# Performance work log

Measured on AMD Instinct MI355X. Metric: run time of the kernel, lower is better.

## Reference

```python
import jax, jax.numpy as jnp
import numpy as np
from jax import lax

# Fixed image shape (H, W) for all images, standard detection resize
H_IMG, W_IMG = 800.0, 1333.0
SCORE_THRESH = 0.05
NMS_THRESH = 0.5
DET_PER_IMG = 100
K_PRE = 2048  # NMS candidate budget per image (after score threshold)
BBOX_XFORM_CLIP = float(np.log(1000.0 / 16.0))
WX, WY, WW, WH = 10.0, 10.0, 5.0, 5.0  # bbox_reg_weights


def setup_inputs() -> dict:
    B, P, C = 8, 2000, 81
    key = jax.random.key(0)
    k1, k2, k3, k4 = jax.random.split(key, 4)
    class_logits = 2.0 * jax.random.normal(k1, (B * P, C), jnp.float32)
    box_regression = 0.5 * jax.random.normal(k2, (B * P, C * 4), jnp.float32)
    # valid proposal boxes inside the image: (x1,y1) + (w,h)
    xy = jax.random.uniform(k3, (B, P, 2), jnp.float32) * jnp.array([W_IMG - 128.0, H_IMG - 128.0], jnp.float32)
    wh = 1.0 + 127.0 * jax.random.uniform(k4, (B, P, 2), jnp.float32)
    proposals = jnp.concatenate([xy, xy + wh], axis=-1)
    return {"class_logits": class_logits, "box_regression": box_regression, "proposals": proposals}


def _decode(rel, boxes):
    # BoxCoder.decode: rel [N, C, 4], boxes [N, 4] -> [N, C, 4]
    w = boxes[:, 2] - boxes[:, 0]
    h = boxes[:, 3] - boxes[:, 1]
    cx = boxes[:, 0] + 0.5 * w
    cy = boxes[:, 1] + 0.5 * h
    dx = rel[..., 0] / WX
    dy = rel[..., 1] / WY
    dw = jnp.minimum(rel[..., 2] / WW, BBOX_XFORM_CLIP)
    dh = jnp.minimum(rel[..., 3] / WH, BBOX_XFORM_CLIP)
    pcx = dx * w[:, None] + cx[:, None]
    pcy = dy * h[:, None] + cy[:, None]
    pw = jnp.exp(dw) * w[:, None]
    ph = jnp.exp(dh) * h[:, None]
    return jnp.stack([pcx - 0.5 * pw, pcy - 0.5 * ph, pcx + 0.5 * pw, pcy + 0.5 * ph], axis=-1)


def _pairwise_iou(b):
    # b: [K, 4] -> [K, K]
    area = jnp.maximum(b[:, 2] - b[:, 0], 0.0) * jnp.maximum(b[:, 3] - b[:, 1], 0.0)
    lt = jnp.maximum(b[:, None, :2], b[None, :, :2])
    rb = jnp.minimum(b[:, None, 2:], b[None, :, 2:])
    wh = jnp.maximum(rb - lt, 0.0)
    inter = wh[..., 0] * wh[..., 1]
    union = area[:, None] + area[None, :] - inter
    return inter / jnp.maximum(union, 1e-9)


def _greedy_nms(boxes, valid):
    # boxes: [K, 4] sorted by score desc; valid: [K] bool. Exact greedy NMS.
    K = boxes.shape[0]
    iou = _pairwise_iou(boxes)
    idx = jnp.arange(K)

    def body(i, keep):
        sup = keep[i] & (iou[i] > NMS_THRESH) & (idx > i)
        return keep & ~sup

    return lax.fori_loop(0, K, body, valid)


def reference(class_logits, box_regression, proposals):
    B, P, _ = proposals.shape
    C = class_logits.shape[-1]
    # decode all class-specific boxes, softmax scores
    rel = box_regression.reshape(-1, C, 4)
    pred = _decode(rel, proposals.reshape(-1, 4)).reshape(B, P, C, 4)
    scores = jax.nn.softmax(class_logits, axis=-1).reshape(B, P, C)
    # drop background class 0
    M = P * (C - 1)
    boxes = pred[:, :, 1:, :].reshape(B, M, 4)
    scores = scores[:, :, 1:].reshape(B, M)
    labels = jnp.broadcast_to(jnp.arange(1, C)[None, None, :], (B, P, C - 1)).reshape(B, M)
    # clip to image
    x1 = jnp.clip(boxes[..., 0], 0.0, W_IMG)
    y1 = jnp.clip(boxes[..., 1], 0.0, H_IMG)
    x2 = jnp.clip(boxes[..., 2], 0.0, W_IMG)
    y2 = jnp.clip(boxes[..., 3], 0.0, H_IMG)
    boxes = jnp.stack([x1, y1, x2, y2], axis=-1)
    # score threshold + remove_small_boxes(min_size=0.01), as a validity mask
    valid = (scores > SCORE_THRESH) & ((x2 - x1) >= 0.01) & ((y2 - y1) >= 0.01)
    masked = jnp.where(valid, scores, -1.0)
    # top-K candidates per image (sorted desc -> NMS visiting order)
    top_s, top_i = lax.top_k(masked, K_PRE)
    top_b = jnp.take_along_axis(boxes, top_i[..., None], axis=1)
    top_l = jnp.take_along_axis(labels, top_i, axis=1)
    top_v = top_s > 0.0
    # batched_nms: per-class coordinate offsets so classes never overlap
    off = top_l.astype(jnp.float32) * (jnp.maximum(W_IMG, H_IMG) + 1.0)
    keep = jax.vmap(_greedy_nms)(top_b + off[..., None], top_v)
    final = jnp.where(keep, top_s, -1.0)
    det_s, det_i = lax.top_k(final, DET_PER_IMG)
    det_b = jnp.take_along_axis(top_b, det_i[..., None], axis=1)
    det_l = jnp.take_along_axis(top_l, det_i, axis=1)
    det_valid = det_s > 0.0  # padding slots have score -1
    return det_b, det_s, det_l, det_valid
```

## Files before the change

### kernel.cpp

```cpp
#include <hip/hip_runtime.h>
#include <cstdint>
#include <cstddef>

typedef unsigned long long u64;

constexpr int Bn   = 8;
constexpr int Pn   = 2000;
constexpr int Cn   = 81;
constexpr int CM1  = 80;
constexpr int KPRE = 2048;
constexpr int NDET = 100;
constexpr int SECP = 8;
constexpr int NSEC2 = Pn / SECP;
constexpr int SSLOT = 160;
constexpr int CAP  = 4096;
constexpr int NBINS = 5632;
constexpr int BINOFF = (122 << 10);
constexpr float W_IMG = 1333.0f;
constexpr float H_IMG = 800.0f;
constexpr float XFORM_CLIP = 4.135166556742356f;
constexpr float NMS_OFF = 1334.0f;

constexpr size_t OFF_HIST = 0;
constexpr size_t ZERO_BYTES = (size_t)Bn * NBINS * 4;
constexpr size_t OFF_SL   = ZERO_BYTES;
constexpr size_t OFF_SC   = OFF_SL + (size_t)Bn * NSEC2 * SSLOT * 8;
constexpr size_t OFF_CANDA = OFF_SC + (size_t)Bn * NSEC2 * 4;

__device__ __forceinline__ void decode_clip(const float4 rv, float w, float h,
                                            float cx, float cy, float out[4]) {
  float dx = rv.x / 10.0f;
  float dy = rv.y / 10.0f;
  float dw = fminf(rv.z / 5.0f, XFORM_CLIP);
  float dh = fminf(rv.w / 5.0f, XFORM_CLIP);
  float pcx = dx * w + cx;
  float pcy = dy * h + cy;
  float pw = expf(dw) * w;
  float ph = expf(dh) * h;
  out[0] = fminf(fmaxf(pcx - 0.5f * pw, 0.0f), W_IMG);
  out[1] = fminf(fmaxf(pcy - 0.5f * ph, 0.0f), H_IMG);
  out[2] = fminf(fmaxf(pcx + 0.5f * pw, 0.0f), W_IMG);
  out[3] = fminf(fmaxf(pcy + 0.5f * ph, 0.0f), H_IMG);
}

__device__ __forceinline__ int score_bin(unsigned bits) {
  int bin = (int)(bits >> 13) - BINOFF;
  return min(max(bin, 0), NBINS - 1);
}

__device__ __forceinline__ void key_decode(u64 key, int b,
                                           const float* __restrict__ reg,
                                           const float* __restrict__ props,
                                           float bx[4], int& label, float& sc) {
  sc = __uint_as_float((unsigned)(key >> 32));
  bx[0] = bx[1] = bx[2] = bx[3] = 0.0f;
  label = 0;
  if (key != 0ull) {
    int m = (int)(0xFFFFFFFFu - (unsigned)key);
    int p = m / CM1;
    int c = m - p * CM1 + 1;
    int nidx = b * Pn + p;
    const float4 pb = *reinterpret_cast<const float4*>(props + (size_t)nidx * 4);
    float w = pb.z - pb.x, h = pb.w - pb.y;
    float cx = pb.x + 0.5f * w, cy = pb.y + 0.5f * h;
    float4 rv = *reinterpret_cast<const float4*>(reg + (size_t)nidx * (Cn * 4) + c * 4);
    decode_clip(rv, w, h, cx, cy, bx);
    label = c;
  }
}

__global__ __launch_bounds__(256) void
k1_score(const float* __restrict__ logits, const float* __restrict__ reg,
         const float* __restrict__ props, u64* __restrict__ slices,
         int* __restrict__ scnt, int* __restrict__ hist) {
  int blk = blockIdx.x, t = threadIdx.x, lane = t & 63, wv = t >> 6;
  int b = blk / NSEC2, sec = blk % NSEC2;
  __shared__ u64 cbuf[SSLOT];
  __shared__ int cnt_sh;
  if (t == 0) cnt_sh = 0;
  __syncthreads();
  int* hrow = hist + (size_t)b * NBINS;

  #pragma unroll
  for (int pp = wv; pp < SECP; pp += 4) {
    int p = sec * SECP + pp;
    int wid = b * Pn + p;
    const float* lg = logits + (size_t)wid * Cn;
    float x0 = lg[lane];
    float x1 = (lane < Cn - 64) ? lg[64 + lane] : -3.4e38f;
    float mx = fmaxf(x0, x1);
    for (int m = 32; m; m >>= 1) mx = fmaxf(mx, __shfl_xor(mx, m, 64));
    float e0 = expf(x0 - mx);
    float e1 = (lane < Cn - 64) ? expf(x1 - mx) : 0.0f;
    float ssum = e0 + e1;
    for (int m = 32; m; m >>= 1) ssum += __shfl_xor(ssum, m, 64);

    const float4 pb = *reinterpret_cast<const float4*>(props + (size_t)wid * 4);
    float w = pb.z - pb.x, h = pb.w - pb.y;
    float cx = pb.x + 0.5f * w, cy = pb.y + 0.5f * h;
    const float* rrow = reg + (size_t)wid * (Cn * 4);

    u64 key0 = 0ull, key1 = 0ull;
    if (lane >= 1) {
      float sc = e0 / ssum;
      if (sc > 0.05f) {
        float4 rv = *reinterpret_cast<const float4*>(rrow + lane * 4);
        float bx[4];
        decode_clip(rv, w, h, cx, cy, bx);
        if ((bx[2] - bx[0] >= 0.01f) && (bx[3] - bx[1] >= 0.01f)) {
          unsigned m = (unsigned)(p * CM1 + (lane - 1));
          key0 = ((u64)__float_as_uint(sc) << 32) | (0xFFFFFFFFu - m);
        }
      }
    }
    if (lane < Cn - 64) {
      int c = 64 + lane;
      float sc = e1 / ssum;
      if (sc > 0.05f) {
        float4 rv = *reinterpret_cast<const float4*>(rrow + c * 4);
        float bx[4];
        decode_clip(rv, w, h, cx, cy, bx);
        if ((bx[2] - bx[0] >= 0.01f) && (bx[3] - bx[1] >= 0.01f)) {
          unsigned m = (unsigned)(p * CM1 + (c - 1));
          key1 = ((u64)__float_as_uint(sc) << 32) | (0xFFFFFFFFu - m);
        }
      }
    }
    u64 bal0 = __ballot(key0 != 0ull);
    u64 bal1 = __ballot(key1 != 0ull);
    int tot = __popcll(bal0) + __popcll(bal1);
    if (tot) {
      int base = 0;
      if (lane == 0) base = atomicAdd(&cnt_sh, tot);
      base = __shfl(base, 0, 64);
      int r0 = __popcll(bal0 & ((1ull << lane) - 1ull));
      int r1 = __popcll(bal0) + __popcll(bal1 & ((1ull << lane) - 1ull));
      if (key0) {
        cbuf[base + r0] = key0;
        atomicAdd(&hrow[score_bin((unsigned)(key0 >> 32))], 1);
      }
      if (key1) {
        cbuf[base + r1] = key1;
        atomicAdd(&hrow[score_bin((unsigned)(key1 >> 32))], 1);
      }
    }
  }
  __syncthreads();
  int n = cnt_sh;
  for (int i = t; i < n; i += 256) slices[(size_t)blk * SSLOT + i] = cbuf[i];
  if (t == 0) scnt[blk] = n;
}

__global__ __launch_bounds__(1024) void
k2c_compact(const int* __restrict__ hist, const u64* __restrict__ slices,
            const int* __restrict__ scnt, u64* __restrict__ candA) {
  int b = blockIdx.x, t = threadIdx.x, lane = t & 63, wv = t >> 6;
  __shared__ int partial[256];
  __shared__ int sufAfter[256];
  __shared__ int lcnt[NSEC2];
  __shared__ int tmax_sh, cnt_sh;
  const int CH = NBINS / 256;
  const int* hrow = hist + (size_t)b * NBINS;

  if (t == 0) { tmax_sh = 0; cnt_sh = 0; }
  if (t < 256) {
    int lo = t * CH, hi = lo + CH;
    int s = 0;
    for (int i = lo; i < hi; i++) s += hrow[i];
    partial[t] = s;
  }
  if (t < NSEC2) lcnt[t] = scnt[b * NSEC2 + t];
  __syncthreads();
  if (t < 256) sufAfter[t] = partial[t];
  __syncthreads();
  for (int s = 1; s < 256; s <<= 1) {
    int y = 0;
    if (t < 256 && t + s < 256) y = sufAfter[t + s];
    __syncthreads();
    if (t < 256) sufAfter[t] += y;
    __syncthreads();
  }
  if (t < 256) {
    int lo = t * CH, hi = lo + CH;
    int cum = (t + 1 < 256) ? sufAfter[t + 1] : 0;
    int cand = -1;
    for (int i = hi - 1; i >= lo; i--) {
      cum += hrow[i];
      if (cum >= KPRE) { cand = i; break; }
    }
    if (cand >= 0) atomicMax(&tmax_sh, cand);
  }
  __syncthreads();
  int T = tmax_sh;

  for (int sec = wv; sec < NSEC2; sec += 16) {
    int n = lcnt[sec];
    const u64* sl = slices + (size_t)(b * NSEC2 + sec) * SSLOT;
    for (int i0 = 0; i0 < n; i0 += 64) {
      int i = i0 + lane;
      u64 key = (i < n) ? sl[i] : 0ull;
      bool pass = key && (score_bin((unsigned)(key >> 32)) >= T);
      u64 bal = __ballot(pass);
      int tot = __popcll(bal);
      if (tot) {
        int base = 0;
        if (lane == 0) base = atomicAdd(&cnt_sh, tot);
        base = __shfl(base, 0, 64);
        int rank = __popcll(bal & ((1ull << lane) - 1ull));
        int pos = base + rank;
        if (pass && pos < CAP) candA[(size_t)b * CAP + pos] = key;
      }
    }
  }
  __syncthreads();
  for (int i = min(cnt_sh, CAP) + t; i < CAP; i += 1024)
    candA[(size_t)b * CAP + i] = 0ull;
}

__global__ __launch_bounds__(256) void
k4a_chunk(u64* __restrict__ candA) {
  __shared__ u64 sk[512];
  int blk = blockIdx.x, t = threadIdx.x;
  int b = blk >> 3, ch = blk & 7;
  int base = ch * 512;
  #pragma unroll
  for (int i = t; i < 512; i += 256) sk[i] = candA[(size_t)b * CAP + base + i];
  __syncthreads();
  for (int k = 2; k <= 512; k <<= 1) {
    for (int j = k >> 1; j > 0; j >>= 1) {
      #pragma unroll
      for (int i = t; i < 512; i += 256) {
        int ixj = i ^ j;
        if (ixj > i) {
          u64 a = sk[i], c2 = sk[ixj];
          bool dir = ((i & k) == 0);
          if ((a < c2) == dir) { sk[i] = c2; sk[ixj] = a; }
        }
      }
      __syncthreads();
    }
  }
  #pragma unroll
  for (int i = t; i < 512; i += 256)
    candA[(size_t)b * CAP + base + i] = sk[i];
}

template <int CHV>
__device__ __forceinline__ void mp_round(u64* buf, int base, int nA, int nB,
                                         int outLen, int tid) {
  const u64* A = buf + base;
  const u64* B = buf + base + nA;
  int d = tid * CHV;
  u64 rg[CHV];
  int cnt = 0;
  if (d < outLen) {
    int lo = max(0, d - nB), hi = min(d, nA);
    while (lo < hi) {
      int mid = (lo + hi) >> 1;
      if (A[mid] >= B[d - 1 - mid]) lo = mid + 1; else hi = mid;
    }
    int i = lo, j = d - lo;
    for (int e = 0; e < CHV && d + e < outLen; e++) {
      u64 v;
      if (j >= nB || (i < nA && A[i] >= B[j])) v = A[i++];
      else v = B[j++];
      rg[cnt++] = v;
    }
  }
  __syncthreads();
  for (int e = 0; e < cnt; e++) buf[base + d + e] = rg[e];
  __syncthreads();
}

__global__ __launch_bounds__(1024) void
k5_merge_nms(u64* __restrict__ candA, const float* __restrict__ reg,
             const float* __restrict__ props, float* __restrict__ out) {
  int b = blockIdx.x, t = threadIdx.x, lane = t & 63, w = t >> 6;
  __shared__ u64 bufA[CAP];
  __shared__ u64 maskb[256][4];
  __shared__ u64 keepw[KPRE / 64];
  __shared__ int accI[NDET];
  __shared__ int kcnt_sh;
  float4* obox = (float4*)bufA;

  #pragma unroll
  for (int s = 0; s < 4; s++) {
    int i = t + s * 1024;
    bufA[i] = candA[(size_t)b * CAP + i];
  }
  __syncthreads();
  mp_round<4>(bufA, (t >> 8) * 1024, 512, 512, 1024, t & 255);
  mp_round<4>(bufA, (t >> 9) * 2048, 1024, 1024, 2048, t & 511);
  mp_round<2>(bufA, 0, 2048, 2048, 2048, t);

  u64 k0 = bufA[t], k1 = bufA[t + 1024];
  candA[(size_t)b * CAP + t] = k0;
  candA[(size_t)b * CAP + t + 1024] = k1;
  {
    u64 bal = __ballot(k0 != 0ull);
    if (lane == 0) keepw[w] = bal;
    bal = __ballot(k1 != 0ull);
    if (lane == 0) keepw[16 + w] = bal;
  }
  __syncthreads();
  #pragma unroll
  for (int s = 0; s < 2; s++) {
    int j = t + s * 1024;
    u64 key = s ? k1 : k0;
    float bx[4]; int label; float sc;
    key_decode(key, b, reg, props, bx, label, sc);
    float off = (float)label * NMS_OFF;
    obox[j] = make_float4(bx[0] + off, bx[1] + off, bx[2] + off, bx[3] + off);
  }
  __syncthreads();

  int kcount = 0;
  for (int w0 = 0; w0 < KPRE && kcount < NDET; w0 += 256) {
    if (w0 > 0 && kcount > 0) {
      if (t < 256) {
        int j = w0 + t;
        u64 kwv = keepw[j >> 6];
        bool alive = (kwv >> (j & 63)) & 1ull;
        if (alive) {
          float4 jb = obox[j];
          float jar = fmaxf(jb.z - jb.x, 0.0f) * fmaxf(jb.w - jb.y, 0.0f);
          for (int a = 0; a < kcount; a++) {
            float4 ab = obox[accI[a]];
            float ix1 = fmaxf(ab.x, jb.x), iy1 = fmaxf(ab.y, jb.y);
            float ix2 = fminf(ab.z, jb.z), iy2 = fminf(ab.w, jb.w);
            float iw = fmaxf(ix2 - ix1, 0.0f), ih = fmaxf(iy2 - iy1, 0.0f);
            float inter = iw * ih;
            if (inter > 0.0f) {
              float aar = fmaxf(ab.z - ab.x, 0.0f) * fmaxf(ab.w - ab.y, 0.0f);
              float iou = inter / fmaxf(aar + jar - inter, 1e-9f);
              if (iou > 0.5f) { alive = false; break; }
            }
          }
        }
        u64 bal = __ballot(alive);
        if (lane == 0) keepw[(w0 >> 6) + (t >> 6)] = bal;
      }
      __syncthreads();
    }
    {
      int r = t >> 2, wd = t & 3;
      int rgp = w0 + r;
      bool ralive = (keepw[rgp >> 6] >> (rgp & 63)) & 1ull;
      float4 rb = obox[rgp];
      float rar = fmaxf(rb.z - rb.x, 0.0f) * fmaxf(rb.w - rb.y, 0.0f);
      u64 m = 0;
      if (ralive) {
        int cb0 = w0 + wd * 64;
        for (int jj = 0; jj < 64; jj++) {
          int cg = cb0 + jj;
          float4 cb = obox[cg];
          float ix1 = fmaxf(rb.x, cb.x), iy1 = fmaxf(rb.y, cb.y);
          float ix2 = fminf(rb.z, cb.z), iy2 = fminf(rb.w, cb.w);
          float iw = fmaxf(ix2 - ix1, 0.0f), ih = fmaxf(iy2 - iy1, 0.0f);
          float inter = iw * ih;
          if (inter > 0.0f && cg > rgp) {
            float car = fmaxf(cb.z - cb.x, 0.0f) * fmaxf(cb.w - cb.y, 0.0f);
            float iou = inter / fmaxf(rar + car - inter, 1e-9f);
            if (iou > 0.5f) m |= (1ull << jj);
          }
        }
      }
      maskb[r][wd] = m;
    }
    __syncthreads();
    if (w == 0) {
      u64 kw0 = keepw[(w0 >> 6) + 0];
      u64 kw1 = keepw[(w0 >> 6) + 1];
      u64 kw2 = keepw[(w0 >> 6) + 2];
      u64 kw3 = keepw[(w0 >> 6) + 3];
      int kc = kcount;
      #pragma unroll
      for (int wq = 0; wq < 4; wq++) {
        u64 cw = (wq == 0) ? kw0 : (wq == 1) ? kw1 : (wq == 2) ? kw2 : kw3;
        if (cw == 0ull) continue;
        for (int rb0 = 0; rb0 < 64 && kc < NDET; rb0 += 4) {
          u64 gbits = (cw >> rb0) & 0xFull;
          int r = wq * 64 + rb0;
          u64 rm0a = maskb[r][0],   rm0b = maskb[r][1],   rm0c = maskb[r][2],   rm0d = maskb[r][3];
          u64 rm1a = maskb[r+1][0], rm1b = maskb[r+1][1], rm1c = maskb[r+1][2], rm1d = maskb[r+1][3];
          u64 rm2a = maskb[r+2][0], rm2b = maskb[r+2][1], rm2c = maskb[r+2][2], rm2d = maskb[r+2][3];
          u64 rm3a = maskb[r+3][0], rm3b = maskb[r+3][1], rm3c = maskb[r+3][2], rm3d = maskb[r+3][3];
          if (gbits == 0ull) continue;
          #pragma unroll
          for (int d = 0; d < 4; d++) {
            u64 cwq = (wq == 0) ? kw0 : (wq == 1) ? kw1 : (wq == 2) ? kw2 : kw3;
            if ((cwq >> (rb0 + d)) & 1ull) {
              if (lane == 0) accI[kc] = w0 + r + d;
              kc++;
              if (kc >= NDET) break;
              u64 ma = (d == 0) ? rm0a : (d == 1) ? rm1a : (d == 2) ? rm2a : rm3a;
              u64 mb = (d == 0) ? rm0b : (d == 1) ? rm1b : (d == 2) ? rm2b : rm3b;
              u64 mc = (d == 0) ? rm0c : (d == 1) ? rm1c : (d == 2) ? rm2c : rm3c;
              u64 md = (d == 0) ? rm0d : (d == 1) ? rm1d : (d == 2) ? rm2d : rm3d;
              kw0 &= ~ma; kw1 &= ~mb; kw2 &= ~mc; kw3 &= ~md;
            }
          }
          cw = (wq == 0) ? kw0 : (wq == 1) ? kw1 : (wq == 2) ? kw2 : kw3;
        }
      }
      if (lane == 0) {
        keepw[(w0 >> 6) + 0] = kw0;
        keepw[(w0 >> 6) + 1] = kw1;
        keepw[(w0 >> 6) + 2] = kw2;
        keepw[(w0 >> 6) + 3] = kw3;
        kcnt_sh = kc;
      }
    }
    __syncthreads();
    kcount = kcnt_sh;
  }

  if (t == 0 && kcount < NDET) {
    int run = kcount;
    for (int wq = 0; wq < KPRE / 64 && run < NDET; wq++) {
      u64 nk = ~keepw[wq];
      while (nk && run < NDET) {
        int bit2 = __ffsll((long long)nk) - 1;
        nk &= nk - 1;
        accI[run++] = wq * 64 + bit2;
      }
    }
  }
  __syncthreads();

  if (t < NDET) {
    int k = accI[t];
    bool kept = t < kcount;
    u64 key = candA[(size_t)b * CAP + k];
    float bx[4]; int label; float sc;
    key_decode(key, b, reg, props, bx, label, sc);
    int oi = b * NDET + t;
    out[(size_t)oi * 4 + 0] = bx[0];
    out[(size_t)oi * 4 + 1] = bx[1];
    out[(size_t)oi * 4 + 2] = bx[2];
    out[(size_t)oi * 4 + 3] = bx[3];
    out[Bn * NDET * 4 + oi] = kept ? sc : -1.0f;
    out[Bn * NDET * 5 + oi] = (float)label;
    out[Bn * NDET * 6 + oi] = kept ? 1.0f : 0.0f;
  }
}

extern "C" void kernel_launch(void* const* d_in, const int* in_sizes, int n_in,
                              void* d_out, int out_size, void* d_ws, size_t ws_size,
                              hipStream_t stream) {
  const float* logits = (const float*)d_in[0];
  const float* reg    = (const float*)d_in[1];
  const float* props  = (const float*)d_in[2];
  float* out = (float*)d_out;
  char* ws = (char*)d_ws;

  int* hist   = (int*)(ws + OFF_HIST);
  u64* slices = (u64*)(ws + OFF_SL);
  int* scnt   = (int*)(ws + OFF_SC);
  u64* candA  = (u64*)(ws + OFF_CANDA);

  hipMemsetAsync(ws + OFF_HIST, 0, ZERO_BYTES, stream);
  k1_score<<<Bn * NSEC2, 256, 0, stream>>>(logits, reg, props, slices, scnt, hist);
  k2c_compact<<<Bn, 1024, 0, stream>>>(hist, slices, scnt, candA);
  k4a_chunk<<<Bn * 8, 256, 0, stream>>>(candA);
  k5_merge_nms<<<Bn, 1024, 0, stream>>>(candA, reg, props, out);
}
```

Measured before the change: 138.5 us.

## Fuse compaction, chunk sort, and merge/NMS into one per-image kernel

Merges the compaction kernel, the 512-chunk bitonic sort kernel and the merge+NMS kernel into a single 1024-thread block per image that keeps candidates in shared memory. This removes two kernel launches and the global round trips of the candidate array between stages. The chunk sort now runs only over chunks that hold candidates. In exchange the sort runs on just 8 blocks instead of 64, so there is less parallelism for that phase.

```diff
diff --git a/kernel.cpp b/kernel.cpp
--- a/kernel.cpp
+++ b/kernel.cpp
@@ -151,17 +151,54 @@
   if (t == 0) scnt[blk] = n;
 }
 
+template <int CHV>
+__device__ __forceinline__ void mp_round(u64* buf, int base, int nA, int nB,
+                                         int outLen, int tid) {
+  const u64* A = buf + base;
+  const u64* B = buf + base + nA;
+  int d = tid * CHV;
+  u64 rg[CHV];
+  int cnt = 0;
+  if (d < outLen) {
+    int lo = max(0, d - nB), hi = min(d, nA);
+    while (lo < hi) {
+      int mid = (lo + hi) >> 1;
+      if (A[mid] >= B[d - 1 - mid]) lo = mid + 1; else hi = mid;
+    }
+    int i = lo, j = d - lo;
+    for (int e = 0; e < CHV && d + e < outLen; e++) {
+      u64 v;
+      if (j >= nB || (i < nA && A[i] >= B[j])) v = A[i++];
+      else v = B[j++];
+      rg[cnt++] = v;
+    }
+  }
+  __syncthreads();
+  for (int e = 0; e < cnt; e++) buf[base + d + e] = rg[e];
+  __syncthreads();
+}
+
 __global__ __launch_bounds__(1024) void
-k2c_compact(const int* __restrict__ hist, const u64* __restrict__ slices,
-            const int* __restrict__ scnt, u64* __restrict__ candA) {
-  int b = blockIdx.x, t = threadIdx.x, lane = t & 63, wv = t >> 6;
+k2_fused(const int* __restrict__ hist, const u64* __restrict__ slices,
+         const int* __restrict__ scnt, u64* __restrict__ candA,
+         const float* __restrict__ reg, const float* __restrict__ props,
+         float* __restrict__ out) {
+  int b = blockIdx.x, t = threadIdx.x, lane = t & 63, w = t >> 6;
+  __shared__ u64 bufA[CAP];
+  __shared__ u64 maskb[256][4];
+  __shared__ u64 keepw[KPRE / 64];
+  __shared__ int accI[NDET];
+  __shared__ int kcnt_sh;
   __shared__ int partial[256];
   __shared__ int sufAfter[256];
   __shared__ int lcnt[NSEC2];
   __shared__ int tmax_sh, cnt_sh;
+  float4* obox = (float4*)bufA;
+
+  for (int i = t; i < CAP; i += 1024) bufA[i] = 0ull;
+
   const int CH = NBINS / 256;
   const int* hrow = hist + (size_t)b * NBINS;
-
   if (t == 0) { tmax_sh = 0; cnt_sh = 0; }
   if (t < 256) {
     int lo = t * CH, hi = lo + CH;
@@ -193,7 +230,7 @@
   __syncthreads();
   int T = tmax_sh;
 
-  for (int sec = wv; sec < NSEC2; sec += 16) {
+  for (int sec = w; sec < NSEC2; sec += 16) {
     int n = lcnt[sec];
     const u64* sl = slices + (size_t)(b * NSEC2 + sec) * SSLOT;
     for (int i0 = 0; i0 < n; i0 += 64) {
@@ -208,87 +245,30 @@
         base = __shfl(base, 0, 64);
         int rank = __popcll(bal & ((1ull << lane) - 1ull));
         int pos = base + rank;
-        if (pass && pos < CAP) candA[(size_t)b * CAP + pos] = key;
-      }
-    }
-  }
-  __syncthreads();
-  for (int i = min(cnt_sh, CAP) + t; i < CAP; i += 1024)
-    candA[(size_t)b * CAP + i] = 0ull;
-}
-
-__global__ __launch_bounds__(256) void
-k4a_chunk(u64* __restrict__ candA) {
-  __shared__ u64 sk[512];
-  int blk = blockIdx.x, t = threadIdx.x;
-  int b = blk >> 3, ch = blk & 7;
-  int base = ch * 512;
-  #pragma unroll
-  for (int i = t; i < 512; i += 256) sk[i] = candA[(size_t)b * CAP + base + i];
-  __syncthreads();
+        if (pass && pos < CAP) bufA[pos] = key;
+      }
+    }
+  }
+  __syncthreads();
+  int cnt = min(cnt_sh, CAP);
+  int nch = (cnt + 511) >> 9;
+  int lim = nch << 9;
+
   for (int k = 2; k <= 512; k <<= 1) {
     for (int j = k >> 1; j > 0; j >>= 1) {
-      #pragma unroll
-      for (int i = t; i < 512; i += 256) {
-        int ixj = i ^ j;
-        if (ixj > i) {
-          u64 a = sk[i], c2 = sk[ixj];
-          bool dir = ((i & k) == 0);
-          if ((a < c2) == dir) { sk[i] = c2; sk[ixj] = a; }
+      for (int i = t; i < lim; i += 1024) {
+        int l = i & 511, cb = i & ~511;
+        int lx = l ^ j;
+        if (lx > l) {
+          u64 a = bufA[cb | l], c2 = bufA[cb | lx];
+          bool dir = ((l & k) == 0);
+          if ((a < c2) == dir) { bufA[cb | l] = c2; bufA[cb | lx] = a; }
         }
       }
       __syncthreads();
     }
   }
-  #pragma unroll
-  for (int i = t; i < 512; i += 256)
-    candA[(size_t)b * CAP + base + i] = sk[i];
-}
-
-template <int CHV>
-__device__ __forceinline__ void mp_round(u64* buf, int base, int nA, int nB,
-                                         int outLen, int tid) {
-  const u64* A = buf + base;
-  const u64* B = buf + base + nA;
-  int d = tid * CHV;
-  u64 rg[CHV];
-  int cnt = 0;
-  if (d < outLen) {
-    int lo = max(0, d - nB), hi = min(d, nA);
-    while (lo < hi) {
-      int mid = (lo + hi) >> 1;
-      if (A[mid] >= B[d - 1 - mid]) lo = mid + 1; else hi = mid;
-    }
-    int i = lo, j = d - lo;
-    for (int e = 0; e < CHV && d + e < outLen; e++) {
-      u64 v;
-      if (j >= nB || (i < nA && A[i] >= B[j])) v = A[i++];
-      else v = B[j++];
-      rg[cnt++] = v;
-    }
-  }
-  __syncthreads();
-  for (int e = 0; e < cnt; e++) buf[base + d + e] = rg[e];
-  __syncthreads();
-}
-
-__global__ __launch_bounds__(1024) void
-k5_merge_nms(u64* __restrict__ candA, const float* __restrict__ reg,
-             const float* __restrict__ props, float* __restrict__ out) {
-  int b = blockIdx.x, t = threadIdx.x, lane = t & 63, w = t >> 6;
-  __shared__ u64 bufA[CAP];
-  __shared__ u64 maskb[256][4];
-  __shared__ u64 keepw[KPRE / 64];
-  __shared__ int accI[NDET];
-  __shared__ int kcnt_sh;
-  float4* obox = (float4*)bufA;
-
-  #pragma unroll
-  for (int s = 0; s < 4; s++) {
-    int i = t + s * 1024;
-    bufA[i] = candA[(size_t)b * CAP + i];
-  }
-  __syncthreads();
+
   mp_round<4>(bufA, (t >> 8) * 1024, 512, 512, 1024, t & 255);
   mp_round<4>(bufA, (t >> 9) * 2048, 1024, 1024, 2048, t & 511);
   mp_round<2>(bufA, 0, 2048, 2048, 2048, t);
@@ -461,7 +441,5 @@
 
   hipMemsetAsync(ws + OFF_HIST, 0, ZERO_BYTES, stream);
   k1_score<<<Bn * NSEC2, 256, 0, stream>>>(logits, reg, props, slices, scnt, hist);
-  k2c_compact<<<Bn, 1024, 0, stream>>>(hist, slices, scnt, candA);
-  k4a_chunk<<<Bn * 8, 256, 0, stream>>>(candA);
-  k5_merge_nms<<<Bn, 1024, 0, stream>>>(candA, reg, props, out);
-}
+  k2_fused<<<Bn, 1024, 0, stream>>>(hist, slices, scnt, candA, reg, props, out);
+}
```

Result: slower. 144.4 us (+4.2%).
